# Kernel optimization log

Measured on AMD Instinct MI355X. Metric: run time of the kernel, lower is better.

Reference implementation:

```python
import jax, jax.numpy as jnp
import numpy as np

N_TILE = 50000
N_POI = 50000
E = 200000
IN_F = 128
HID = 256
OUT = 256
HEADS = 8
NEG_SLOPE = 0.2


def gatv2(hs, hd, src, dst, Wsrc, bsrc, Wdst, bdst, attn, n_dst):
    """DGL GATv2Conv: per-edge LeakyReLU(fs_u + fd_v) attention, edge-softmax over
    incoming edges of each dst node, attention-weighted sum of source features.
    Returns (n_dst, H*D) (already flattened, matching .flatten(1))."""
    H, D = attn.shape
    fs = (hs @ Wsrc + bsrc).reshape(-1, H, D)  # (Ns, H, D)
    fd = (hd @ Wdst + bdst).reshape(-1, H, D)  # (Nd, H, D)
    e = jax.nn.leaky_relu(fs[src] + fd[dst], NEG_SLOPE)       # (E, H, D)
    logits = jnp.einsum('ehd,hd->eh', e, attn)                # (E, H)
    # segment softmax over destination neighborhoods
    mx = jax.ops.segment_max(logits, dst, num_segments=n_dst)  # (Nd, H)
    ex = jnp.exp(logits - mx[dst])
    den = jax.ops.segment_sum(ex, dst, num_segments=n_dst)
    alpha = ex / den[dst]                                      # (E, H)
    out = jax.ops.segment_sum(fs[src] * alpha[:, :, None], dst, num_segments=n_dst)
    return out.reshape(n_dst, H * D)


def hetero_layer(ht, hp, Wsrc, bsrc, Wdst, bdst, attn, idx, mean_agg):
    src_road, dst_road, src_tb, dst_tb, src_ct, dst_ct = idx
    m_road = gatv2(ht, ht, src_road, dst_road, Wsrc[0], bsrc[0], Wdst[0], bdst[0], attn[0], N_TILE)
    m_tb = gatv2(hp, ht, src_tb, dst_tb, Wsrc[1], bsrc[1], Wdst[1], bdst[1], attn[1], N_TILE)
    m_ct = gatv2(ht, hp, src_ct, dst_ct, Wsrc[2], bsrc[2], Wdst[2], bdst[2], attn[2], N_POI)
    tile = (m_road + m_tb) * (0.5 if mean_agg else 1.0)  # cross-relation sum/mean
    poi = m_ct  # single relation: sum == mean
    return jax.nn.relu(tile), jax.nn.relu(poi)


def _params(key, fan_in, fan_out, heads, dhead):
    ks = jax.random.split(key, 5)
    s = 1.0 / np.sqrt(fan_in)
    return (jax.random.normal(ks[0], (3, fan_in, fan_out), jnp.float32) * s,
            jnp.zeros((3, fan_out), jnp.float32),
            jax.random.normal(ks[1], (3, fan_in, fan_out), jnp.float32) * s,
            jnp.zeros((3, fan_out), jnp.float32),
            jax.random.normal(ks[2], (3, heads, dhead), jnp.float32) * s)


def setup_inputs() -> dict:
    key = jax.random.key(0)
    ks = jax.random.split(key, 12)
    inp = {
        'x_tile': jax.random.normal(ks[0], (N_TILE, IN_F), jnp.float32),
        'x_poi': jax.random.normal(ks[1], (N_POI, IN_F), jnp.float32),
        'src_road': jax.random.randint(ks[2], (E,), 0, N_TILE, jnp.int32),
        'dst_road': jax.random.randint(ks[3], (E,), 0, N_TILE, jnp.int32),
        'src_tb': jax.random.randint(ks[4], (E,), 0, N_POI, jnp.int32),
        'dst_tb': jax.random.randint(ks[5], (E,), 0, N_TILE, jnp.int32),
        'src_ct': jax.random.randint(ks[6], (E,), 0, N_TILE, jnp.int32),
        'dst_ct': jax.random.randint(ks[7], (E,), 0, N_POI, jnp.int32),
    }
    D = HID // HEADS
    for i, (fi, fo) in enumerate([(IN_F, HID), (HID, HID), (HID, OUT)]):
        Ws, bs, Wd, bd, at = _params(ks[8 + i], fi, fo, HEADS, fo // HEADS)
        inp[f'W_src_{i}'] = Ws; inp[f'b_src_{i}'] = bs
        inp[f'W_dst_{i}'] = Wd; inp[f'b_dst_{i}'] = bd
        inp[f'attn_{i}'] = at
    return inp


def reference(x_tile, x_poi, src_road, dst_road, src_tb, dst_tb, src_ct, dst_ct,
              W_src_0, b_src_0, W_dst_0, b_dst_0, attn_0,
              W_src_1, b_src_1, W_dst_1, b_dst_1, attn_1,
              W_src_2, b_src_2, W_dst_2, b_dst_2, attn_2):
    idx = (src_road, dst_road, src_tb, dst_tb, src_ct, dst_ct)
    ht, hp = hetero_layer(x_tile, x_poi, W_src_0, b_src_0, W_dst_0, b_dst_0, attn_0, idx, mean_agg=False)
    ht, hp = hetero_layer(ht, hp, W_src_1, b_src_1, W_dst_1, b_dst_1, attn_1, idx, mean_agg=True)
    ht, hp = hetero_layer(ht, hp, W_src_2, b_src_2, W_dst_2, b_dst_2, attn_2, idx, mean_agg=False)
    return ht, hp
```

## Files before the change

kernel.cpp:

```cpp
#include <hip/hip_runtime.h>
#include <hip/hip_bf16.h>

typedef __hip_bfloat16 bf16;

#define NT 50000
#define NP 50000
#define NE 200000
#define HH 8
#define DD 32
#define CC 256
#define NBLK 196

typedef short s8v __attribute__((ext_vector_type(8)));
typedef float f4v __attribute__((ext_vector_type(4)));

__device__ __forceinline__ float bu2f(unsigned short u) {
  return __uint_as_float(((unsigned)u) << 16);
}
__device__ __forceinline__ unsigned short f2bu(float x) {
  bf16 b = __float2bfloat16(x);
  return *(unsigned short*)&b;
}

__device__ __forceinline__ void gload_lds16(const void* g, void* l) {
  __builtin_amdgcn_global_load_lds(
      (const __attribute__((address_space(1))) void*)g,
      (__attribute__((address_space(3))) void*)l, 16, 0, 0);
}

__global__ __launch_bounds__(256) void cvt2_f2b(
    const float* __restrict__ a, const float* __restrict__ b,
    bf16* __restrict__ oa, bf16* __restrict__ ob, int n) {
  int i = blockIdx.x * 256 + threadIdx.x;
  if (i >= n) return;
  if (blockIdx.y == 0) oa[i] = __float2bfloat16(a[i]);
  else                 ob[i] = __float2bfloat16(b[i]);
}

struct WtArgs {
  const float* Ws[3]; const float* Wd[3];
  bf16* W1[3]; bf16* W2[3];
};
__global__ __launch_bounds__(256) void wt_cvt_all(WtArgs a) {
  int l = blockIdx.z, y = blockIdx.y;
  int K = (l == 0) ? 128 : 256;
  int idx = blockIdx.x * 256 + threadIdx.x;
  if (idx >= 256 * K) return;
  int n = idx / K, k = idx - n * K;
  const float* W; bf16* D; int dn;
  if (y == 0)      { W = a.Ws[l];                       D = a.W1[l]; dn = n; }
  else if (y == 1) { W = a.Wd[l];                       D = a.W1[l]; dn = n + 256; }
  else if (y == 2) { W = a.Wd[l] + (size_t)1 * K * 256; D = a.W1[l]; dn = n + 512; }
  else if (y == 3) { W = a.Ws[l] + (size_t)2 * K * 256; D = a.W1[l]; dn = n + 768; }
  else if (y == 4) { W = a.Ws[l] + (size_t)1 * K * 256; D = a.W2[l]; dn = n; }
  else             { W = a.Wd[l] + (size_t)2 * K * 256; D = a.W2[l]; dn = n + 256; }
  D[(size_t)dn * K + k] = __float2bfloat16(W[(size_t)k * 256 + n]);
}

struct BiArgs {
  const float* bs[3]; const float* bd[3];
  float* b1; float* b2;
};
__global__ __launch_bounds__(256) void bias_cat(BiArgs a) {
  int l = blockIdx.y, y = blockIdx.x;
  int n = threadIdx.x;
  float v;
  if (y == 0)      v = a.bs[l][n];
  else if (y == 1) v = a.bd[l][n];
  else if (y == 2) v = a.bd[l][256 + n];
  else if (y == 3) v = a.bs[l][512 + n];
  else if (y == 4) v = a.bs[l][256 + n];
  else             v = a.bd[l][512 + n];
  if (y < 4) a.b1[l * 1024 + y * 256 + n] = v;
  else       a.b2[l * 512 + (y - 4) * 256 + n] = v;
}

__global__ __launch_bounds__(256) void zero_i(int* __restrict__ p, int n) {
  int i = blockIdx.x * 256 + threadIdx.x;
  if (i < n) p[i] = 0;
}

__global__ __launch_bounds__(256) void hist3(
    const int* __restrict__ d0, const int* __restrict__ d1,
    const int* __restrict__ d2, int* __restrict__ deg) {
  int r = blockIdx.y;
  int e = blockIdx.x * 256 + threadIdx.x;
  if (e >= NE) return;
  const int* d = (r == 0) ? d0 : (r == 1) ? d1 : d2;
  atomicAdd(&deg[r * NT + d[e]], 1);
}

__global__ __launch_bounds__(256) void scan_s1(const int* __restrict__ deg,
                                               int* __restrict__ bsum) {
  __shared__ int buf[256];
  int r = blockIdx.y, b = blockIdx.x, t = threadIdx.x;
  int idx = b * 256 + t;
  buf[t] = (idx < NT) ? deg[r * NT + idx] : 0;
  __syncthreads();
  for (int s = 128; s > 0; s >>= 1) {
    if (t < s) buf[t] += buf[t + s];
    __syncthreads();
  }
  if (t == 0) bsum[r * NBLK + b] = buf[0];
}

__global__ __launch_bounds__(256) void scan_s2(
    const int* __restrict__ bsum, int* __restrict__ boff,
    int* __restrict__ offs) {
  __shared__ int buf[256];
  int t = threadIdx.x;
  for (int r = 0; r < 3; r++) {
    int v = (t < NBLK) ? bsum[r * NBLK + t] : 0;
    buf[t] = v;
    __syncthreads();
    for (int s = 1; s < 256; s <<= 1) {
      int u = (t >= s) ? buf[t - s] : 0;
      __syncthreads();
      buf[t] += u;
      __syncthreads();
    }
    if (t < NBLK) boff[r * NBLK + t] = buf[t] - v;
    if (t == 255) offs[(size_t)r * (NT + 1) + NT] = buf[255];
    __syncthreads();
  }
}

__global__ __launch_bounds__(256) void scan_s3(
    const int* __restrict__ deg, const int* __restrict__ boff,
    int* __restrict__ offs, int* __restrict__ cursor) {
  __shared__ int buf[256];
  int r = blockIdx.y, b = blockIdx.x, t = threadIdx.x;
  int idx = b * 256 + t;
  int v = (idx < NT) ? deg[r * NT + idx] : 0;
  buf[t] = v;
  __syncthreads();
  for (int s = 1; s < 256; s <<= 1) {
    int u = (t >= s) ? buf[t - s] : 0;
    __syncthreads();
    buf[t] += u;
    __syncthreads();
  }
  int o = boff[r * NBLK + b] + buf[t] - v;
  if (idx < NT) {
    offs[(size_t)r * (NT + 1) + idx] = o;
    cursor[r * NT + idx] = o;
  }
}

__global__ __launch_bounds__(256) void fill3(
    const int* __restrict__ d0, const int* __restrict__ d1,
    const int* __restrict__ d2, const int* __restrict__ s0,
    const int* __restrict__ s1, const int* __restrict__ s2,
    int* __restrict__ cursor, int* __restrict__ csrc) {
  int r = blockIdx.y;
  int e = blockIdx.x * 256 + threadIdx.x;
  if (e >= NE) return;
  const int* d = (r == 0) ? d0 : (r == 1) ? d1 : d2;
  const int* s = (r == 0) ? s0 : (r == 1) ? s1 : s2;
  int p = atomicAdd(&cursor[r * NT + d[e]], 1);
  csrc[(size_t)r * NE + p] = s[e];
}

__global__ __launch_bounds__(512, 2) void gemm256(
    const bf16* __restrict__ A1, const bf16* __restrict__ B1t,
    const float* __restrict__ bias1, bf16* __restrict__ C1,
    const bf16* __restrict__ A2, const bf16* __restrict__ B2t,
    const float* __restrict__ bias2, bf16* __restrict__ C2,
    int M, int K, int q8, int r8) {
  __shared__ short LDS[2][2][8192];
  int bid = blockIdx.x;
  int xcd = bid & 7, pos = bid >> 3;
  int wg = (xcd < r8 ? xcd * (q8 + 1) : r8 * (q8 + 1) + (xcd - r8) * q8) + pos;
  int bm = wg / 6, bn = wg - bm * 6;

  const bf16* A; const bf16* Bt; const float* bias; bf16* Cout; int Ncols, col0;
  if (bn < 4) { A = A1; Bt = B1t + (size_t)bn * 256 * K; bias = bias1; Cout = C1; Ncols = 1024; col0 = bn * 256; }
  else { A = A2; Bt = B2t + (size_t)(bn - 4) * 256 * K; bias = bias2; Cout = C2; Ncols = 512; col0 = (bn - 4) * 256; }

  int t = threadIdx.x;
  int lane = t & 63;
  int wid = t >> 6;
  int wm = wid >> 2, wn = wid & 3;
  int row0 = bm * 256;
  int wbase = t & ~63;

  f4v acc[4][8] = {};

  const bf16* Abase = A + (size_t)row0 * K;

  auto stage = [&](int buf, int kt) {
    int kofs = kt * 32;
    #pragma unroll
    for (int j = 0; j < 2; j++) {
      int s = j * 512 + t;
      int row = s >> 2, ch = s & 3;
      int sch = ch ^ ((row >> 1) & 3);
      gload_lds16(Abase + (size_t)row * K + kofs + sch * 8,
                  &LDS[buf][0][(j * 512 + wbase) * 8]);
    }
    #pragma unroll
    for (int j = 0; j < 2; j++) {
      int s = j * 512 + t;
      int row = s >> 2, ch = s & 3;
      int sch = ch ^ ((row >> 1) & 3);
      gload_lds16(Bt + (size_t)row * K + kofs + sch * 8,
                  &LDS[buf][1][(j * 512 + wbase) * 8]);
    }
  };

  int nk = K / 32;
  stage(0, 0);
  stage(1, 1);
  asm volatile("s_waitcnt vmcnt(4)" ::: "memory");
  __builtin_amdgcn_s_barrier();
  __builtin_amdgcn_sched_barrier(0);

  int cur = 0;
  for (int kt = 0; kt < nk; kt++) {
    int ch = lane >> 4;
    int rr = lane & 15;
    s8v af[4], bfv[8];
    #pragma unroll
    for (int i = 0; i < 4; i++) {
      int row = wn * 64 + i * 16 + rr;
      af[i] = *(const s8v*)&LDS[cur][1][(row * 4 + (ch ^ ((row >> 1) & 3))) * 8];
    }
    #pragma unroll
    for (int j = 0; j < 8; j++) {
      int row = wm * 128 + j * 16 + rr;
      bfv[j] = *(const s8v*)&LDS[cur][0][(row * 4 + (ch ^ ((row >> 1) & 3))) * 8];
    }
    asm volatile("s_waitcnt lgkmcnt(0)" ::: "memory");
    __builtin_amdgcn_s_barrier();
    __builtin_amdgcn_sched_barrier(0);
    bool staged = (kt + 2 < nk);
    if (staged) stage(cur, kt + 2);
    #pragma unroll
    for (int i = 0; i < 4; i++)
      #pragma unroll
      for (int j = 0; j < 8; j++)
        acc[i][j] = __builtin_amdgcn_mfma_f32_16x16x32_bf16(
            af[i], bfv[j], acc[i][j], 0, 0, 0);
    if (kt + 1 < nk) {
      if (staged) {
        asm volatile("s_waitcnt vmcnt(4)" ::: "memory");
      } else {
        asm volatile("s_waitcnt vmcnt(0)" ::: "memory");
      }
      __builtin_amdgcn_s_barrier();
      __builtin_amdgcn_sched_barrier(0);
    }
    cur ^= 1;
  }

  short* CL = &LDS[0][0][0];
  unsigned short* Cu = (unsigned short*)Cout;
  int q = lane >> 4, rr = lane & 15;
  #pragma unroll
  for (int p = 0; p < 2; p++) {
    __syncthreads();
    if (wm == p) {
      #pragma unroll
      for (int j = 0; j < 8; j++) {
        int row = j * 16 + rr;
        #pragma unroll
        for (int i = 0; i < 4; i++) {
          int n0 = wn * 64 + i * 16 + q * 4;
          float4 bv = *(const float4*)(bias + col0 + n0);
          ushort4 v = make_ushort4(f2bu(acc[i][j][0] + bv.x),
                                   f2bu(acc[i][j][1] + bv.y),
                                   f2bu(acc[i][j][2] + bv.z),
                                   f2bu(acc[i][j][3] + bv.w));
          int g = n0 >> 2;
          int slot = (g >> 1) ^ (row & 15);
          *(ushort4*)(CL + row * 256 + slot * 8 + (g & 1) * 4) = v;
        }
      }
    }
    __syncthreads();
    {
      int row = t >> 2, seg = t & 3;
      int grow = row0 + p * 128 + row;
      if (grow < M) {
        #pragma unroll
        for (int j2 = 0; j2 < 8; j2++) {
          int slot = j2 * 4 + seg;
          int slot_s = slot ^ (row & 15);
          s8v v = *(const s8v*)(CL + row * 256 + slot_s * 8);
          *(s8v*)&Cu[(size_t)grow * Ncols + col0 + slot * 8] = v;
        }
      }
    }
  }
}

__device__ __forceinline__ float edge_logit(
    ushort4 u, float d0, float d1, float d2, float d3, float4 at,
    float& f0, float& f1, float& f2, float& f3) {
  f0 = bu2f(u.x); f1 = bu2f(u.y); f2 = bu2f(u.z); f3 = bu2f(u.w);
  float t0 = f0 + d0; t0 = t0 > 0.f ? t0 : 0.2f * t0;
  float t1 = f1 + d1; t1 = t1 > 0.f ? t1 : 0.2f * t1;
  float t2 = f2 + d2; t2 = t2 > 0.f ? t2 : 0.2f * t2;
  float t3 = f3 + d3; t3 = t3 > 0.f ? t3 : 0.2f * t3;
  float lg = t0 * at.x + t1 * at.y + t2 * at.z + t3 * at.w;
  lg += __shfl_xor(lg, 1);
  lg += __shfl_xor(lg, 2);
  lg += __shfl_xor(lg, 4);
  return lg;
}

__device__ __forceinline__ float4 gat_pass(
    int e0, int e1, const int* __restrict__ csrc,
    const unsigned short* __restrict__ base, size_t stride,
    float d0, float d1, float d2, float d3, float4 at) {
  float m = -1e30f, den = 0.f;
  float a0 = 0.f, a1 = 0.f, a2 = 0.f, a3 = 0.f;
  int e = e0;
  for (; e + 4 <= e1; e += 4) {
    int s0 = csrc[e], s1 = csrc[e + 1], s2 = csrc[e + 2], s3 = csrc[e + 3];
    ushort4 u0 = *(const ushort4*)(base + (size_t)s0 * stride);
    ushort4 u1 = *(const ushort4*)(base + (size_t)s1 * stride);
    ushort4 u2 = *(const ushort4*)(base + (size_t)s2 * stride);
    ushort4 u3 = *(const ushort4*)(base + (size_t)s3 * stride);
    float f0, f1, f2, f3, g0, g1, g2, g3, h0, h1, h2, h3, i0, i1, i2, i3;
    float lg0 = edge_logit(u0, d0, d1, d2, d3, at, f0, f1, f2, f3);
    float lg1 = edge_logit(u1, d0, d1, d2, d3, at, g0, g1, g2, g3);
    float lg2 = edge_logit(u2, d0, d1, d2, d3, at, h0, h1, h2, h3);
    float lg3 = edge_logit(u3, d0, d1, d2, d3, at, i0, i1, i2, i3);
    float mn = fmaxf(fmaxf(fmaxf(lg0, lg1), fmaxf(lg2, lg3)), m);
    float c = __expf(m - mn);
    float x0 = __expf(lg0 - mn);
    float x1 = __expf(lg1 - mn);
    float x2 = __expf(lg2 - mn);
    float x3 = __expf(lg3 - mn);
    den = den * c + x0 + x1 + x2 + x3;
    a0 = a0 * c + x0 * f0 + x1 * g0 + x2 * h0 + x3 * i0;
    a1 = a1 * c + x0 * f1 + x1 * g1 + x2 * h1 + x3 * i1;
    a2 = a2 * c + x0 * f2 + x1 * g2 + x2 * h2 + x3 * i2;
    a3 = a3 * c + x0 * f3 + x1 * g3 + x2 * h3 + x3 * i3;
    m = mn;
  }
  for (; e < e1; ++e) {
    int s0 = csrc[e];
    ushort4 u0 = *(const ushort4*)(base + (size_t)s0 * stride);
    float f0, f1, f2, f3;
    float lg0 = edge_logit(u0, d0, d1, d2, d3, at, f0, f1, f2, f3);
    float mn = fmaxf(m, lg0);
    float c = __expf(m - mn);
    float x0 = __expf(lg0 - mn);
    den = den * c + x0;
    a0 = a0 * c + x0 * f0;
    a1 = a1 * c + x0 * f1;
    a2 = a2 * c + x0 * f2;
    a3 = a3 * c + x0 * f3;
    m = mn;
  }
  float inv = (den > 0.f) ? 1.f / den : 0.f;
  return make_float4(a0 * inv, a1 * inv, a2 * inv, a3 * inv);
}

__global__ __launch_bounds__(256) void node_gat_all(
    const int* __restrict__ offs, const int* __restrict__ csrc,
    const bf16* __restrict__ F1, const bf16* __restrict__ F2,
    const float* __restrict__ attnL, float scale,
    bf16* __restrict__ ht_n, bf16* __restrict__ hp_n,
    float* __restrict__ outT, float* __restrict__ outP) {
  __shared__ float rbuf[2][64][4];
  int gw = blockIdx.x * 4 + (threadIdx.x >> 6);
  int lane = threadIdx.x & 63;
  int off = (lane >> 3) * DD + (lane & 7) * 4;
  const unsigned short* F1u = (const unsigned short*)F1;
  const unsigned short* F2u = (const unsigned short*)F2;

  if (gw < 2 * NT) {
    int node = gw >> 1;
    int pass = gw & 1;
    int pair = threadIdx.x >> 7;

    const int* po = pass ? (offs + (NT + 1)) : offs;
    const int* pc = pass ? (csrc + NE) : csrc;
    const unsigned short* pb = pass ? (F2u + off) : (F1u + off);
    size_t stride = pass ? 512 : 1024;
    int udofs = pass ? 512 : 256;
    ushort4 ud = *(const ushort4*)(F1u + (size_t)node * 1024 + udofs + off);
    float4 at = *(const float4*)(attnL + (pass ? 256 : 0) + off);

    float4 r = gat_pass(po[node], po[node + 1], pc, pb, stride,
                        bu2f(ud.x), bu2f(ud.y), bu2f(ud.z), bu2f(ud.w), at);

    if (pass) {
      rbuf[pair][lane][0] = r.x; rbuf[pair][lane][1] = r.y;
      rbuf[pair][lane][2] = r.z; rbuf[pair][lane][3] = r.w;
    }
    __syncthreads();
    if (!pass) {
      float v0 = (r.x + rbuf[pair][lane][0]) * scale; v0 = v0 > 0.f ? v0 : 0.f;
      float v1 = (r.y + rbuf[pair][lane][1]) * scale; v1 = v1 > 0.f ? v1 : 0.f;
      float v2 = (r.z + rbuf[pair][lane][2]) * scale; v2 = v2 > 0.f ? v2 : 0.f;
      float v3 = (r.w + rbuf[pair][lane][3]) * scale; v3 = v3 > 0.f ? v3 : 0.f;
      size_t base = (size_t)node * CC + off;
      if (ht_n)
        *(ushort4*)((unsigned short*)ht_n + base) =
            make_ushort4(f2bu(v0), f2bu(v1), f2bu(v2), f2bu(v3));
      if (outT) *(float4*)(outT + base) = make_float4(v0, v1, v2, v3);
    }
  } else {
    int w = gw - 2 * NT;
    const int* offsC = offs + 2 * (NT + 1);
    ushort4 ud = *(const ushort4*)(F2u + (size_t)w * 512 + 256 + off);
    float4 at = *(const float4*)(attnL + 512 + off);
    float4 r = gat_pass(offsC[w], offsC[w + 1], csrc + 2 * (size_t)NE,
                        F1u + 768 + off, 1024,
                        bu2f(ud.x), bu2f(ud.y), bu2f(ud.z), bu2f(ud.w), at);

    float v0 = r.x > 0.f ? r.x : 0.f;
    float v1 = r.y > 0.f ? r.y : 0.f;
    float v2 = r.z > 0.f ? r.z : 0.f;
    float v3 = r.w > 0.f ? r.w : 0.f;

    size_t base = (size_t)w * CC + off;
    if (hp_n)
      *(ushort4*)((unsigned short*)hp_n + base) =
          make_ushort4(f2bu(v0), f2bu(v1), f2bu(v2), f2bu(v3));
    if (outP) *(float4*)(outP + base) = make_float4(v0, v1, v2, v3);
  }
}

extern "C" void kernel_launch(void* const* d_in, const int* in_sizes, int n_in,
                              void* d_out, int out_size, void* d_ws, size_t ws_size,
                              hipStream_t stream) {
  const float* x_tile = (const float*)d_in[0];
  const float* x_poi  = (const float*)d_in[1];
  const int* src_road = (const int*)d_in[2];
  const int* dst_road = (const int*)d_in[3];
  const int* src_tb   = (const int*)d_in[4];
  const int* dst_tb   = (const int*)d_in[5];
  const int* src_ct   = (const int*)d_in[6];
  const int* dst_ct   = (const int*)d_in[7];
  const float* Wsrc[3] = {(const float*)d_in[8],  (const float*)d_in[13], (const float*)d_in[18]};
  const float* bsrc[3] = {(const float*)d_in[9],  (const float*)d_in[14], (const float*)d_in[19]};
  const float* Wdst[3] = {(const float*)d_in[10], (const float*)d_in[15], (const float*)d_in[20]};
  const float* bdst[3] = {(const float*)d_in[11], (const float*)d_in[16], (const float*)d_in[21]};
  const float* attn[3] = {(const float*)d_in[12], (const float*)d_in[17], (const float*)d_in[22]};

  bf16* hbuf = (bf16*)d_ws;
  bf16* ht2[2] = {hbuf, hbuf + (size_t)NT * CC};
  bf16* hp2[2] = {hbuf + 2 * (size_t)NT * CC, hbuf + 3 * (size_t)NT * CC};
  bf16* F1 = hbuf + 4 * (size_t)NT * CC;
  bf16* F2 = F1 + (size_t)NT * 1024;
  int* offs = (int*)(F2 + (size_t)NT * 512);
  int* deg  = offs + 3 * (NT + 1);
  int* csrc = deg + 3 * NT;
  int* bsum = csrc + (size_t)3 * NE;
  int* boff = bsum + 3 * NBLK;
  uintptr_t wp = ((uintptr_t)(boff + 3 * NBLK) + 63) & ~(uintptr_t)63;
  bf16* W1c[3], *W2c[3];
  {
    bf16* w = (bf16*)wp;
    for (int l = 0; l < 3; l++) {
      int K = (l == 0) ? 128 : 256;
      W1c[l] = w; w += (size_t)1024 * K;
      W2c[l] = w; w += (size_t)512 * K;
    }
    wp = (uintptr_t)w;
  }
  float* b1 = (float*)((wp + 63) & ~(uintptr_t)63);
  float* b2 = b1 + 3 * 1024;

  {
    dim3 gc((NT * 128 + 255) / 256, 2);
    cvt2_f2b<<<gc, 256, 0, stream>>>(x_tile, x_poi, ht2[0], hp2[0], NT * 128);
  }

  {
    WtArgs wa;
    BiArgs ba;
    for (int l = 0; l < 3; l++) {
      wa.Ws[l] = Wsrc[l]; wa.Wd[l] = Wdst[l];
      wa.W1[l] = W1c[l];  wa.W2[l] = W2c[l];
      ba.bs[l] = bsrc[l]; ba.bd[l] = bdst[l];
    }
    ba.b1 = b1; ba.b2 = b2;
    dim3 gw(256, 6, 3);
    wt_cvt_all<<<gw, 256, 0, stream>>>(wa);
    dim3 gb(6, 3);
    bias_cat<<<gb, 256, 0, stream>>>(ba);
  }

  zero_i<<<(3 * NT + 255) / 256, 256, 0, stream>>>(deg, 3 * NT);
  {
    dim3 ge((NE + 255) / 256, 3);
    hist3<<<ge, 256, 0, stream>>>(dst_road, dst_tb, dst_ct, deg);
    dim3 gn(NBLK, 3);
    scan_s1<<<gn, 256, 0, stream>>>(deg, bsum);
    scan_s2<<<1, 256, 0, stream>>>(bsum, boff, offs);
    scan_s3<<<gn, 256, 0, stream>>>(deg, boff, offs, deg);
    fill3<<<ge, 256, 0, stream>>>(dst_road, dst_tb, dst_ct,
                                  src_road, src_tb, src_ct, deg, csrc);
  }

  int cb = 0;
  for (int l = 0; l < 3; l++) {
    int K = (l == 0) ? 128 : 256;
    bf16* ht_c = ht2[cb], *hp_c = hp2[cb];
    bf16* ht_n = (l == 2) ? nullptr : ht2[cb ^ 1];
    bf16* hp_n = (l == 2) ? nullptr : hp2[cb ^ 1];
    float st = (l == 1) ? 0.5f : 1.0f;
    float* outT = (l == 2) ? (float*)d_out : nullptr;
    float* outP = (l == 2) ? ((float*)d_out + (size_t)NT * CC) : nullptr;

    int NW = NBLK * 6, q8 = NW / 8, r8 = NW % 8;
    gemm256<<<NW, 512, 0, stream>>>(
        ht_c, W1c[l], b1 + l * 1024, F1,
        hp_c, W2c[l], b2 + l * 512,  F2,
        NT, K, q8, r8);

    node_gat_all<<<(2 * NT + NP) / 4, 256, 0, stream>>>(
        offs, csrc, F1, F2, attn[l], st, ht_n, hp_n, outT, outP);

    cb ^= 1;
  }
}
```

Measured before the change: 551.1 us.

## Load weight fragments directly from global into registers, stage only A via LDS

The GEMM now keeps only the activation tile in LDS and loads each wave's weight (Bt) fragments straight from global memory into registers, prefetching the next k-step into a second register set. The pipeline drops from two stages ahead with fine-grained vmcnt waits to one stage ahead with plain __syncthreads. This halves LDS traffic and LDS reads per step, but adds redundant global loads of B across waves and shallower prefetch, which may expose memory latency.

```diff
diff --git a/kernel.cpp b/kernel.cpp
--- a/kernel.cpp
+++ b/kernel.cpp
@@ -167,7 +167,7 @@
     const bf16* __restrict__ A2, const bf16* __restrict__ B2t,
     const float* __restrict__ bias2, bf16* __restrict__ C2,
     int M, int K, int q8, int r8) {
-  __shared__ short LDS[2][2][8192];
+  __shared__ short LDS[32768];
   int bid = blockIdx.x;
   int xcd = bid & 7, pos = bid >> 3;
   int wg = (xcd < r8 ? xcd * (q8 + 1) : r8 * (q8 + 1) + (xcd - r8) * q8) + pos;
@@ -188,74 +188,59 @@
 
   const bf16* Abase = A + (size_t)row0 * K;
 
-  auto stage = [&](int buf, int kt) {
+  auto stageA = [&](int buf, int kt) {
     int kofs = kt * 32;
     #pragma unroll
     for (int j = 0; j < 2; j++) {
       int s = j * 512 + t;
-      int row = s >> 2, ch = s & 3;
-      int sch = ch ^ ((row >> 1) & 3);
+      int row = s >> 2, ch2 = s & 3;
+      int sch = ch2 ^ ((row >> 1) & 3);
       gload_lds16(Abase + (size_t)row * K + kofs + sch * 8,
-                  &LDS[buf][0][(j * 512 + wbase) * 8]);
-    }
-    #pragma unroll
-    for (int j = 0; j < 2; j++) {
-      int s = j * 512 + t;
-      int row = s >> 2, ch = s & 3;
-      int sch = ch ^ ((row >> 1) & 3);
-      gload_lds16(Bt + (size_t)row * K + kofs + sch * 8,
-                  &LDS[buf][1][(j * 512 + wbase) * 8]);
+                  &LDS[buf * 8192 + (j * 512 + wbase) * 8]);
     }
   };
 
+  int ch = lane >> 4;
+  int rr = lane & 15;
+  const bf16* Bfrag = Bt + (size_t)(wn * 64 + rr) * K + ch * 8;
+
   int nk = K / 32;
-  stage(0, 0);
-  stage(1, 1);
-  asm volatile("s_waitcnt vmcnt(4)" ::: "memory");
-  __builtin_amdgcn_s_barrier();
-  __builtin_amdgcn_sched_barrier(0);
+  s8v af[4], afn[4];
+  stageA(0, 0);
+  #pragma unroll
+  for (int i = 0; i < 4; i++)
+    af[i] = *(const s8v*)(Bfrag + (size_t)i * 16 * K);
+  __syncthreads();
 
   int cur = 0;
   for (int kt = 0; kt < nk; kt++) {
-    int ch = lane >> 4;
-    int rr = lane & 15;
-    s8v af[4], bfv[8];
-    #pragma unroll
-    for (int i = 0; i < 4; i++) {
-      int row = wn * 64 + i * 16 + rr;
-      af[i] = *(const s8v*)&LDS[cur][1][(row * 4 + (ch ^ ((row >> 1) & 3))) * 8];
-    }
+    if (kt + 1 < nk) {
+      stageA(cur ^ 1, kt + 1);
+      #pragma unroll
+      for (int i = 0; i < 4; i++)
+        afn[i] = *(const s8v*)(Bfrag + (size_t)i * 16 * K + (kt + 1) * 32);
+    }
+    s8v bfv[8];
     #pragma unroll
     for (int j = 0; j < 8; j++) {
       int row = wm * 128 + j * 16 + rr;
-      bfv[j] = *(const s8v*)&LDS[cur][0][(row * 4 + (ch ^ ((row >> 1) & 3))) * 8];
-    }
-    asm volatile("s_waitcnt lgkmcnt(0)" ::: "memory");
-    __builtin_amdgcn_s_barrier();
-    __builtin_amdgcn_sched_barrier(0);
-    bool staged = (kt + 2 < nk);
-    if (staged) stage(cur, kt + 2);
+      bfv[j] = *(const s8v*)&LDS[cur * 8192 + (row * 4 + (ch ^ ((row >> 1) & 3))) * 8];
+    }
     #pragma unroll
     for (int i = 0; i < 4; i++)
       #pragma unroll
       for (int j = 0; j < 8; j++)
         acc[i][j] = __builtin_amdgcn_mfma_f32_16x16x32_bf16(
             af[i], bfv[j], acc[i][j], 0, 0, 0);
-    if (kt + 1 < nk) {
-      if (staged) {
-        asm volatile("s_waitcnt vmcnt(4)" ::: "memory");
-      } else {
-        asm volatile("s_waitcnt vmcnt(0)" ::: "memory");
-      }
-      __builtin_amdgcn_s_barrier();
-      __builtin_amdgcn_sched_barrier(0);
-    }
+    __syncthreads();
+    #pragma unroll
+    for (int i = 0; i < 4; i++) af[i] = afn[i];
     cur ^= 1;
   }
 
-  short* CL = &LDS[0][0][0];
+  short* CL = &LDS[0];
   unsigned short* Cu = (unsigned short*)Cout;
-  int q = lane >> 4, rr = lane & 15;
+  int q = lane >> 4;
   #pragma unroll
   for (int p = 0; p < 2; p++) {
     __syncthreads();
```

Result: slower. 607.6 us (+10.3%).
